# Kernel tuning notes

Hardware: AMD Instinct MI355X
Metric: run time of the kernel (lower is better)

The kernel has to match this reference:

```python
import jax, jax.numpy as jnp
import numpy as np

MAX_SEQ = 20          # text-token prefix length (config.max_seq_length)
NUM_HEADS = 12        # == num_spatial_relations
HEAD_DIM = 64         # 768 / 12
QUADRANTS = (1, 2, 4, 7, 8, 9)
NEG = -10000.0

BS, N_FEAT, D = 128, 182, 768   # N_FEAT = 20 text + 150 ocr/obj + 12 decode steps
R_OCR_OBJ = 150


def setup_inputs() -> dict:
    key = jax.random.key(0)
    ks = jax.random.split(key, 8)
    hidden_states = jax.random.normal(ks[0], (BS, N_FEAT, D), dtype=jnp.float32)
    attention_mask = jnp.where(
        jax.random.uniform(ks[1], (BS, 1, 1, N_FEAT)) < 0.9, 0.0, NEG
    ).astype(jnp.float32)
    # binary spatial relation adjacency (bs, R, R, 12)
    spatial_adj_matrix = jax.random.randint(
        ks[2], (BS, R_OCR_OBJ, R_OCR_OBJ, NUM_HEADS), 0, 2
    ).astype(jnp.float32)
    scale = 0.02
    Wq = jax.random.normal(ks[3], (D, D), dtype=jnp.float32) * scale
    Wk = jax.random.normal(ks[4], (D, D), dtype=jnp.float32) * scale
    Wv = jax.random.normal(ks[5], (D, D), dtype=jnp.float32) * scale
    bq = jnp.zeros((D,), jnp.float32)
    bk = jnp.zeros((D,), jnp.float32)
    bv = jnp.zeros((D,), jnp.float32)
    return {
        "hidden_states": hidden_states,
        "attention_mask": attention_mask,
        "spatial_adj_matrix": spatial_adj_matrix,
        "Wq": Wq, "bq": bq, "Wk": Wk, "bk": bk, "Wv": Wv, "bv": bv,
    }


def _spatial_additive_mask(spatial_adj_matrix, num_features, dtype):
    """Builds (bs, heads, N, N) additive mask in {0, -10000}, faithful to the
    sequential ones-fill / adjacency-copy / quadrant-zero / (1-m)*-10000 / permute."""
    bs, R = spatial_adj_matrix.shape[0], spatial_adj_matrix.shape[1]
    S = MAX_SEQ
    m = jnp.ones((bs, num_features, num_features, NUM_HEADS), dtype)
    m = m.at[:, S:S + R, S:S + R, :].set(spatial_adj_matrix.astype(dtype))
    for quad in QUADRANTS:  # num_spatial_relations == num_heads, so all head channels
        if quad == 1:
            m = m.at[:, :S, :S, :].set(0.0)
        elif quad == 2:
            m = m.at[:, :S, S:S + R, :].set(0.0)
        elif quad == 4:
            m = m.at[:, S:S + R, :S, :].set(0.0)
        elif quad == 7:
            m = m.at[:, S + R:, :S, :].set(0.0)
        elif quad == 8:
            m = m.at[:, S + R:, S:S + R, :].set(0.0)
        elif quad == 9:
            m = m.at[:, S + R:, S + R:, :].set(0.0)
    return jnp.transpose((1.0 - m) * NEG, (0, 3, 1, 2))  # (bs, H, N, N)


def _heads(x, bs, n):
    return jnp.transpose(x.reshape(bs, n, NUM_HEADS, HEAD_DIM), (0, 2, 1, 3))


def reference(hidden_states, attention_mask, spatial_adj_matrix,
              Wq, bq, Wk, bk, Wv, bv):
    bs, n, _ = hidden_states.shape
    spatial = _spatial_additive_mask(spatial_adj_matrix, n, hidden_states.dtype)
    # combined additive mask in {0, -10000}; attention_mask broadcasts (bs,1,1,N)
    combined = jnp.minimum(attention_mask, spatial)
    # 1.0 where a query row has at least one attendable key, else 0.0
    entity_probs_mask = (jnp.max(combined, axis=-1, keepdims=True) + 10000.0) / 10000.0

    q = _heads(hidden_states @ Wq.T + bq, bs, n)  # (bs, H, N, d)
    k = _heads(hidden_states @ Wk.T + bk, bs, n)
    v = _heads(hidden_states @ Wv.T + bv, bs, n)

    scores = jnp.einsum('bhqd,bhkd->bhqk', q, k) / 8.0 + combined  # sqrt(64)=8
    probs = jax.nn.softmax(scores, axis=-1) * entity_probs_mask
    ctx = jnp.einsum('bhqk,bhkd->bhqd', probs, v)
    ctx = jnp.transpose(ctx, (0, 2, 1, 3)).reshape(bs, n, NUM_HEADS * HEAD_DIM)
    return ctx
```

## Files before the change

### kernel.cpp

```cpp
#include <hip/hip_runtime.h>
#include <hip/hip_bf16.h>

#define NBS   128
#define NF    182
#define NP    192
#define DMODEL 768
#define NH    12
#define HDIM  64
#define SEQT  20
#define ROCR  150

typedef __attribute__((ext_vector_type(4))) float  f32x4;
typedef __attribute__((ext_vector_type(8))) short  s16x8;
typedef __attribute__((ext_vector_type(4))) unsigned int u32x4;
using bf16 = __hip_bfloat16;

#define SB()    __builtin_amdgcn_sched_barrier(0)
#define BAR()   __builtin_amdgcn_s_barrier()

__device__ __forceinline__ void gload_lds16(const void* g, void* l) {
    auto gp = (const __attribute__((address_space(1))) unsigned int*)((unsigned long long)g);
    auto lp = (__attribute__((address_space(3))) unsigned int*)(unsigned int)((unsigned long long)l);
    __builtin_amdgcn_global_load_lds(gp, lp, 16, 0, 0);
}

#define CVT_BLOCKS 9600
__global__ __launch_bounds__(256) void prep(
    const float* __restrict__ hs,
    const float* __restrict__ Wq, const float* __restrict__ Wk, const float* __restrict__ Wv,
    const float* __restrict__ adj,
    bf16* __restrict__ hsb, bf16* __restrict__ Wb2,
    unsigned long long* __restrict__ bits)
{
    __shared__ float tile[ROCR * NH];
    if (blockIdx.x < CVT_BLOCKS) {
        const size_t HT = (size_t)NBS * NF * DMODEL / 8;
        const size_t WT = 3ull * DMODEL * DMODEL / 8;
        size_t i = (size_t)blockIdx.x * 256 + threadIdx.x;
        if (i >= HT + WT) return;
        const float* src; bf16* dst;
        if (i < HT) {
            size_t e = i * 8; src = hs + e; dst = hsb + e;
        } else {
            size_t e = (i - HT) * 8;
            int R = (int)(e / DMODEL), c = (int)(e % DMODEL);
            int h = R / 192, t2 = (R % 192) / 64, r0 = R % 64;
            src = (t2 == 0 ? Wq : t2 == 1 ? Wk : Wv) + (size_t)(h * 64 + r0) * DMODEL + c;
            dst = Wb2 + e;
        }
        float4 a = *reinterpret_cast<const float4*>(src);
        float4 b = *reinterpret_cast<const float4*>(src + 4);
        union { s16x8 v; bf16 h8[8]; } u;
        u.h8[0] = __float2bfloat16(a.x); u.h8[1] = __float2bfloat16(a.y);
        u.h8[2] = __float2bfloat16(a.z); u.h8[3] = __float2bfloat16(a.w);
        u.h8[4] = __float2bfloat16(b.x); u.h8[5] = __float2bfloat16(b.y);
        u.h8[6] = __float2bfloat16(b.z); u.h8[7] = __float2bfloat16(b.w);
        *reinterpret_cast<s16x8*>(dst) = u.v;
    } else {
        const int pb = blockIdx.x - CVT_BLOCKS;
        const int b = pb / ROCR, r = pb - b * ROCR;
        const int tid = threadIdx.x, lane = tid & 63, w = tid >> 6;
        const float* src = adj + ((size_t)b * ROCR + r) * (ROCR * NH);
        for (int i = tid; i < ROCR * NH; i += 256) tile[i] = src[i];
        __syncthreads();
        for (int c = w; c < NH * 3; c += 4) {
            int hh = c / 3, wd = c - hh * 3;
            int k = wd * 64 + lane;
            int j = k - SEQT;
            bool v = false;
            if (j >= 0 && j < ROCR) v = (tile[j * NH + hh] > 0.5f);
            unsigned long long m = __ballot(v);
            if (lane == 0) bits[(((size_t)b * NH + hh) * ROCR + r) * 3 + wd] = m;
        }
    }
}

#define KO2   0
#define VTO2  24576
#define QO3   49152

__global__ __launch_bounds__(256, 2) void fused_qkv_attn(
    const bf16* __restrict__ hsb, const bf16* __restrict__ Wb2,
    const float* __restrict__ bq, const float* __restrict__ bk, const float* __restrict__ bv,
    const float* __restrict__ amask,
    const unsigned long long* __restrict__ bits,
    float* __restrict__ out)
{
    __shared__ char L[73728];
    const int tid  = threadIdx.x;
    const int lane = tid & 63;
    const int wid  = tid >> 6;
    const int wr = wid >> 1, wc = wid & 1;
    const int lm = lane & 15, lg = lane >> 4;

    const int flat = blockIdx.x;
    const int wgid = (flat & 7) * 192 + (flat >> 3);
    const int b = wgid / NH, h = wgid - b * NH;

    float* obase = out + (size_t)b * NF * DMODEL + h * HDIM;

    unsigned long long aw0, aw1, aw2;
    {
        int k0 = lane, k1 = 64 + lane, k2 = 128 + lane;
        aw0 = __ballot(amask[b * NF + k0] == 0.0f);
        aw1 = __ballot(amask[b * NF + k1] == 0.0f);
        aw2 = __ballot((k2 < NF) && (amask[b * NF + k2] == 0.0f));
    }
    for (int i = tid; i < 12 * 64; i += 256)
        obase[(size_t)(170 + (i >> 6)) * DMODEL + (i & 63)] = 0.f;

    const char* gA = (const char*)(hsb + (size_t)b * NF * DMODEL);
    const char* gW = (const char*)(Wb2 + (size_t)h * 192 * DMODEL);

    f32x4 acc[6][6];
    #pragma unroll
    for (int i = 0; i < 6; ++i)
        #pragma unroll
        for (int j = 0; j < 6; ++j) acc[i][j] = (f32x4){0.f, 0.f, 0.f, 0.f};

    const int srow4 = tid >> 2, sch4 = tid & 3;

    auto ST = [&](int kt, int bsel) {
        char* dA = L + bsel * 24576;
        char* dW = dA + 12288;
        #pragma unroll
        for (int it = 0; it < 3; ++it) {
            int row = it * 64 + srow4;
            int lc = sch4 ^ ((row >> 1) & 3);
            size_t go = (size_t)row * 1536 + (size_t)kt * 64 + lc * 16;
            int o = row * 64 + sch4 * 16;
            gload_lds16(gA + go, dA + o);
            gload_lds16(gW + go, dW + o);
        }
    };
    auto CP = [&](int bsel) {
        const char* Ab = L + bsel * 24576;
        const char* Wp = Ab + 12288;
        s16x8 af[6], bf6[6];
        #pragma unroll
        for (int mi = 0; mi < 6; ++mi) {
            int r = 96 * wr + 16 * mi + lm;
            af[mi] = *reinterpret_cast<const s16x8*>(Ab + r * 64 + ((lg ^ ((r >> 1) & 3)) << 4));
        }
        #pragma unroll
        for (int ni = 0; ni < 6; ++ni) {
            int r = 96 * wc + 16 * ni + lm;
            bf6[ni] = *reinterpret_cast<const s16x8*>(Wp + r * 64 + ((lg ^ ((r >> 1) & 3)) << 4));
        }
        __builtin_amdgcn_s_setprio(1);
        #pragma unroll
        for (int mi = 0; mi < 6; ++mi)
            #pragma unroll
            for (int ni = 0; ni < 6; ++ni)
                acc[mi][ni] = __builtin_amdgcn_mfma_f32_16x16x32_bf16(af[mi], bf6[ni], acc[mi][ni], 0, 0, 0);
        __builtin_amdgcn_s_setprio(0);
    };

    ST(0, 0);
    ST(1, 1);
    ST(2, 2);
    for (int t = 0; t < 24; ++t) {
        if (t <= 21)      { asm volatile("s_waitcnt vmcnt(12)" ::: "memory"); }
        else if (t == 22) { asm volatile("s_waitcnt vmcnt(6)"  ::: "memory"); }
        else              { asm volatile("s_waitcnt vmcnt(0)"  ::: "memory"); }
        SB(); BAR(); SB();
        CP(t % 3);
        SB(); BAR();
        if (t + 3 < 24) ST(t + 3, t % 3);
    }
    BAR();

    float bias6[6];
    #pragma unroll
    for (int ni = 0; ni < 6; ++ni) {
        int c = 96 * wc + 16 * ni + lm;
        int whichc = c >> 6, cc = c & 63;
        const float* bp = (whichc == 0) ? bq : (whichc == 1) ? bk : bv;
        bias6[ni] = bp[h * 64 + cc];
    }
    #pragma unroll
    for (int mi = 0; mi < 6; ++mi) {
        #pragma unroll
        for (int ni = 0; ni < 6; ++ni) {
            int c = 96 * wc + 16 * ni + lm;
            int row0 = 96 * wr + 16 * mi + 4 * lg;
            if (c < 64) {
                #pragma unroll
                for (int j = 0; j < 4; ++j) {
                    int row = row0 + j;
                    bf16 hv = __float2bfloat16((acc[mi][ni][j] + bias6[ni]) * 0.125f);
                    *reinterpret_cast<unsigned short*>(L + QO3 + row * 128 + ((2 * c) ^ ((row & 7) << 4))) =
                        *reinterpret_cast<unsigned short*>(&hv);
                }
            } else if (c < 128) {
                int cc = c - 64;
                #pragma unroll
                for (int j = 0; j < 4; ++j) {
                    int row = row0 + j;
                    bf16 hv = __float2bfloat16(acc[mi][ni][j] + bias6[ni]);
                    *reinterpret_cast<unsigned short*>(L + KO2 + row * 128 + ((2 * cc) ^ ((row & 7) << 4))) =
                        *reinterpret_cast<unsigned short*>(&hv);
                }
            } else {
                int d = c - 128;
                if (row0 + 3 < NF) {
                    union { unsigned long long u8; bf16 h[4]; } pk;
                    pk.h[0] = __float2bfloat16(acc[mi][ni][0] + bias6[ni]);
                    pk.h[1] = __float2bfloat16(acc[mi][ni][1] + bias6[ni]);
                    pk.h[2] = __float2bfloat16(acc[mi][ni][2] + bias6[ni]);
                    pk.h[3] = __float2bfloat16(acc[mi][ni][3] + bias6[ni]);
                    *reinterpret_cast<unsigned long long*>(L + VTO2 + d * 384 + ((2 * row0) ^ ((d & 7) << 4))) = pk.u8;
                } else {
                    #pragma unroll
                    for (int j = 0; j < 4; ++j) {
                        int row = row0 + j;
                        if (row < NF) {
                            bf16 hv = __float2bfloat16(acc[mi][ni][j] + bias6[ni]);
                            *reinterpret_cast<unsigned short*>(L + VTO2 + d * 384 + ((2 * row) ^ ((d & 7) << 4))) =
                                *reinterpret_cast<unsigned short*>(&hv);
                        }
                    }
                }
            }
        }
    }
    for (int i = tid; i < 64 * 10; i += 256) {
        int d = i / 10, k2 = NF + (i - d * 10);
        *reinterpret_cast<unsigned short*>(L + VTO2 + d * 384 + ((2 * k2) ^ ((d & 7) << 4))) = 0;
    }
    __syncthreads();

    s16x8 qf[3][2];
    #pragma unroll
    for (int bi = 0; bi < 3; ++bi) {
        int band = wid + 4 * bi;
        int qrow = ((band < 11) ? band * 16 : 0) + lm;
        const char* qb = L + QO3 + qrow * 128;
        int sq = (qrow & 7) << 4;
        qf[bi][0] = *reinterpret_cast<const s16x8*>(qb + ((lg * 16) ^ sq));
        qf[bi][1] = *reinterpret_cast<const s16x8*>(qb + ((64 + lg * 16) ^ sq));
    }

    const unsigned long long* bbase = bits + ((size_t)b * NH + h) * ROCR * 3;
    const unsigned long long DEC = 0xFFFull << 42;

    #pragma unroll
    for (int bi = 0; bi < 3; ++bi) {
        const int band = wid + 4 * bi;
        if (band >= 11) continue;
        const int q0 = band * 16;

        const int qrow = q0 + lm;
        unsigned long long mw0, mw1, mw2;
        if (qrow < SEQT) {
            mw0 = 0; mw1 = 0; mw2 = DEC & aw2;
        } else {
            const unsigned long long* bp = bbase + (size_t)(qrow - SEQT) * 3;
            mw0 = bp[0] & aw0;
            mw1 = bp[1] & aw1;
            mw2 = (bp[2] | DEC) & aw2;
        }

        f32x4 sacc[12];
        #pragma unroll
        for (int t = 0; t < 12; ++t) sacc[t] = (f32x4){0.f, 0.f, 0.f, 0.f};
        #pragma unroll
        for (int t = 0; t < 12; ++t) {
            int key = t * 16 + lm;
            const char* kb = L + KO2 + key * 128;
            int sw = (key & 7) << 4;
            s16x8 kf0 = *reinterpret_cast<const s16x8*>(kb + ((lg * 16) ^ sw));
            s16x8 kf1 = *reinterpret_cast<const s16x8*>(kb + ((64 + lg * 16) ^ sw));
            sacc[t] = __builtin_amdgcn_mfma_f32_16x16x32_bf16(kf0, qf[bi][0], sacc[t], 0, 0, 0);
            sacc[t] = __builtin_amdgcn_mfma_f32_16x16x32_bf16(kf1, qf[bi][1], sacc[t], 0, 0, 0);
        }

        float mx = -3.0e38f;
        #pragma unroll
        for (int t = 0; t < 12; ++t) {
            unsigned long long w = (t < 4) ? mw0 : (t < 8) ? mw1 : mw2;
            #pragma unroll
            for (int j = 0; j < 4; ++j) {
                int sh = ((t & 3) << 4) + 4 * lg + j;
                float s = sacc[t][j];
                s = ((w >> sh) & 1ull) ? s : -3.0e38f;
                sacc[t][j] = s;
                mx = fmaxf(mx, s);
            }
        }
        mx = fmaxf(mx, __shfl_xor(mx, 16));
        mx = fmaxf(mx, __shfl_xor(mx, 32));
        float sum = 0.f;
        #pragma unroll
        for (int t = 0; t < 12; ++t)
            #pragma unroll
            for (int j = 0; j < 4; ++j) {
                float e = (sacc[t][j] > -1.0e37f) ? __expf(sacc[t][j] - mx) : 0.f;
                sacc[t][j] = e;
                sum += e;
            }
        sum += __shfl_xor(sum, 16);
        sum += __shfl_xor(sum, 32);
        float scl = (mx > -1.0e37f) ? 1.0f / sum : 0.f;

        unsigned int p0[12], p1[12];
        #pragma unroll
        for (int t = 0; t < 12; ++t) {
            bf16 b0 = __float2bfloat16(sacc[t][0] * scl);
            bf16 b1 = __float2bfloat16(sacc[t][1] * scl);
            bf16 b2 = __float2bfloat16(sacc[t][2] * scl);
            bf16 b3 = __float2bfloat16(sacc[t][3] * scl);
            p0[t] = (unsigned int)*reinterpret_cast<unsigned short*>(&b0)
                  | ((unsigned int)*reinterpret_cast<unsigned short*>(&b1) << 16);
            p1[t] = (unsigned int)*reinterpret_cast<unsigned short*>(&b2)
                  | ((unsigned int)*reinterpret_cast<unsigned short*>(&b3) << 16);
        }

        f32x4 oacc[4];
        #pragma unroll
        for (int t = 0; t < 4; ++t) oacc[t] = (f32x4){0.f, 0.f, 0.f, 0.f};
        const bool hi = (lg & 1);
        #pragma unroll
        for (int ks = 0; ks < 6; ++ks) {
            unsigned int A0 = p0[2 * ks],     A1 = p1[2 * ks];
            unsigned int B0 = p0[2 * ks + 1], B1 = p1[2 * ks + 1];
            unsigned int u0 = __shfl_xor(A0, 16), u1 = __shfl_xor(A1, 16);
            unsigned int v0 = __shfl_xor(B0, 16), v1 = __shfl_xor(B1, 16);
            unsigned int hA0 = hi ? u0 : A0, hA1 = hi ? u1 : A1;
            unsigned int hA2 = hi ? A0 : u0, hA3 = hi ? A1 : u1;
            unsigned int hB0 = hi ? v0 : B0, hB1 = hi ? v1 : B1;
            unsigned int hB2 = hi ? B0 : v0, hB3 = hi ? B1 : v1;
            unsigned int xA0 = __shfl_xor(hA0, 32), xA1 = __shfl_xor(hA1, 32);
            unsigned int xA2 = __shfl_xor(hA2, 32), xA3 = __shfl_xor(hA3, 32);
            unsigned int xB0 = __shfl_xor(hB0, 32), xB1 = __shfl_xor(hB1, 32);
            unsigned int xB2 = __shfl_xor(hB2, 32), xB3 = __shfl_xor(hB3, 32);
            u32x4 f;
            if (lg == 0)      f = (u32x4){hA0, hA1, hA2, hA3};
            else if (lg == 1) f = (u32x4){xA0, xA1, xA2, xA3};
            else if (lg == 2) f = (u32x4){xB0, xB1, xB2, xB3};
            else              f = (u32x4){hB0, hB1, hB2, hB3};
            s16x8 pa;
            __builtin_memcpy(&pa, &f, 16);
            #pragma unroll
            for (int t2 = 0; t2 < 4; ++t2) {
                int d = t2 * 16 + lm;
                s16x8 vf = *reinterpret_cast<const s16x8*>(L + VTO2 + d * 384 + ((ks * 64 + lg * 16) ^ ((d & 7) << 4)));
                oacc[t2] = __builtin_amdgcn_mfma_f32_16x16x32_bf16(pa, vf, oacc[t2], 0, 0, 0);
            }
        }
        #pragma unroll
        for (int j = 0; j < 4; ++j) {
            int row = q0 + lg * 4 + j;
            if (row < 170) {
                #pragma unroll
                for (int t2 = 0; t2 < 4; ++t2)
                    obase[(size_t)row * DMODEL + t2 * 16 + lm] = oacc[t2][j];
            }
        }
    }
}

extern "C" void kernel_launch(void* const* d_in, const int* in_sizes, int n_in,
                              void* d_out, int out_size, void* d_ws, size_t ws_size,
                              hipStream_t stream)
{
    const float* hs    = (const float*)d_in[0];
    const float* amask = (const float*)d_in[1];
    const float* adj   = (const float*)d_in[2];
    const float* Wq    = (const float*)d_in[3];
    const float* bq    = (const float*)d_in[4];
    const float* Wk    = (const float*)d_in[5];
    const float* bk    = (const float*)d_in[6];
    const float* Wv    = (const float*)d_in[7];
    const float* bv    = (const float*)d_in[8];
    float* out = (float*)d_out;

    char* ws = (char*)d_ws;
    bf16* Wb2 = (bf16*)ws;
    unsigned long long* bits = (unsigned long long*)(ws + 3538944);
    bf16* hsb = (bf16*)(ws + 3538944 + 5529600);

    prep<<<dim3(CVT_BLOCKS + ROCR * NBS), 256, 0, stream>>>(hs, Wq, Wk, Wv, adj, hsb, Wb2, bits);
    fused_qkv_attn<<<dim3(NBS * NH), 256, 0, stream>>>(hsb, Wb2, bq, bk, bv, amask, bits, out);
}
```

Measured before the change: 202.3 us.

## Use 12 waves per block for fused QKV projection and attention

Raises the fused QKV+attention block from 4 to 12 waves (768 threads, 1 block per CU). In the projection GEMM each wave now owns a 48x64 tile in a 4x3 grid, with the column group matching Q, K or V. Each wave loads one row of each staged tile and works one 16-row query band in attention, so there is no loop over three bands. This cuts per-wave accumulator registers and serial work per wave and spreads latency hiding across more waves. The cost is 1 block per CU instead of 2, and one wave sits idle during the attention phase.

```diff
diff --git a/kernel.cpp b/kernel.cpp
--- a/kernel.cpp
+++ b/kernel.cpp
@@ -79,7 +79,7 @@
 #define VTO2  24576
 #define QO3   49152
 
-__global__ __launch_bounds__(256, 2) void fused_qkv_attn(
+__global__ __launch_bounds__(768, 1) void fused_qkv_attn(
     const bf16* __restrict__ hsb, const bf16* __restrict__ Wb2,
     const float* __restrict__ bq, const float* __restrict__ bk, const float* __restrict__ bv,
     const float* __restrict__ amask,
@@ -90,7 +90,7 @@
     const int tid  = threadIdx.x;
     const int lane = tid & 63;
     const int wid  = tid >> 6;
-    const int wr = wid >> 1, wc = wid & 1;
+    const int wr = wid / 3, wc = wid - wr * 3;
     const int lm = lane & 15, lg = lane >> 4;
 
     const int flat = blockIdx.x;
@@ -106,53 +106,47 @@
         aw1 = __ballot(amask[b * NF + k1] == 0.0f);
         aw2 = __ballot((k2 < NF) && (amask[b * NF + k2] == 0.0f));
     }
-    for (int i = tid; i < 12 * 64; i += 256)
-        obase[(size_t)(170 + (i >> 6)) * DMODEL + (i & 63)] = 0.f;
+    obase[(size_t)(170 + (tid >> 6)) * DMODEL + (tid & 63)] = 0.f;
 
     const char* gA = (const char*)(hsb + (size_t)b * NF * DMODEL);
     const char* gW = (const char*)(Wb2 + (size_t)h * 192 * DMODEL);
 
-    f32x4 acc[6][6];
+    f32x4 acc[3][4];
     #pragma unroll
-    for (int i = 0; i < 6; ++i)
-        #pragma unroll
-        for (int j = 0; j < 6; ++j) acc[i][j] = (f32x4){0.f, 0.f, 0.f, 0.f};
-
-    const int srow4 = tid >> 2, sch4 = tid & 3;
+    for (int i = 0; i < 3; ++i)
+        #pragma unroll
+        for (int j = 0; j < 4; ++j) acc[i][j] = (f32x4){0.f, 0.f, 0.f, 0.f};
+
+    const int srow = tid >> 2, sch = tid & 3;
 
     auto ST = [&](int kt, int bsel) {
         char* dA = L + bsel * 24576;
-        char* dW = dA + 12288;
-        #pragma unroll
-        for (int it = 0; it < 3; ++it) {
-            int row = it * 64 + srow4;
-            int lc = sch4 ^ ((row >> 1) & 3);
-            size_t go = (size_t)row * 1536 + (size_t)kt * 64 + lc * 16;
-            int o = row * 64 + sch4 * 16;
-            gload_lds16(gA + go, dA + o);
-            gload_lds16(gW + go, dW + o);
-        }
+        int lc = sch ^ ((srow >> 1) & 3);
+        size_t go = (size_t)srow * 1536 + (size_t)kt * 64 + lc * 16;
+        int o = srow * 64 + sch * 16;
+        gload_lds16(gA + go, dA + o);
+        gload_lds16(gW + go, dA + 12288 + o);
     };
     auto CP = [&](int bsel) {
         const char* Ab = L + bsel * 24576;
         const char* Wp = Ab + 12288;
-        s16x8 af[6], bf6[6];
-        #pragma unroll
-        for (int mi = 0; mi < 6; ++mi) {
-            int r = 96 * wr + 16 * mi + lm;
+        s16x8 af[3], bf4[4];
+        #pragma unroll
+        for (int mi = 0; mi < 3; ++mi) {
+            int r = 48 * wr + 16 * mi + lm;
             af[mi] = *reinterpret_cast<const s16x8*>(Ab + r * 64 + ((lg ^ ((r >> 1) & 3)) << 4));
         }
         #pragma unroll
-        for (int ni = 0; ni < 6; ++ni) {
-            int r = 96 * wc + 16 * ni + lm;
-            bf6[ni] = *reinterpret_cast<const s16x8*>(Wp + r * 64 + ((lg ^ ((r >> 1) & 3)) << 4));
+        for (int ni = 0; ni < 4; ++ni) {
+            int r = 64 * wc + 16 * ni + lm;
+            bf4[ni] = *reinterpret_cast<const s16x8*>(Wp + r * 64 + ((lg ^ ((r >> 1) & 3)) << 4));
         }
         __builtin_amdgcn_s_setprio(1);
         #pragma unroll
-        for (int mi = 0; mi < 6; ++mi)
-            #pragma unroll
-            for (int ni = 0; ni < 6; ++ni)
-                acc[mi][ni] = __builtin_amdgcn_mfma_f32_16x16x32_bf16(af[mi], bf6[ni], acc[mi][ni], 0, 0, 0);
+        for (int mi = 0; mi < 3; ++mi)
+            #pragma unroll
+            for (int ni = 0; ni < 4; ++ni)
+                acc[mi][ni] = __builtin_amdgcn_mfma_f32_16x16x32_bf16(af[mi], bf4[ni], acc[mi][ni], 0, 0, 0);
         __builtin_amdgcn_s_setprio(0);
     };
 
@@ -160,9 +154,9 @@
     ST(1, 1);
     ST(2, 2);
     for (int t = 0; t < 24; ++t) {
-        if (t <= 21)      { asm volatile("s_waitcnt vmcnt(12)" ::: "memory"); }
-        else if (t == 22) { asm volatile("s_waitcnt vmcnt(6)"  ::: "memory"); }
-        else              { asm volatile("s_waitcnt vmcnt(0)"  ::: "memory"); }
+        if (t <= 21)      { asm volatile("s_waitcnt vmcnt(4)" ::: "memory"); }
+        else if (t == 22) { asm volatile("s_waitcnt vmcnt(2)" ::: "memory"); }
+        else              { asm volatile("s_waitcnt vmcnt(0)" ::: "memory"); }
         SB(); BAR(); SB();
         CP(t % 3);
         SB(); BAR();
@@ -170,84 +164,79 @@
     }
     BAR();
 
-    float bias6[6];
-    #pragma unroll
-    for (int ni = 0; ni < 6; ++ni) {
-        int c = 96 * wc + 16 * ni + lm;
-        int whichc = c >> 6, cc = c & 63;
-        const float* bp = (whichc == 0) ? bq : (whichc == 1) ? bk : bv;
-        bias6[ni] = bp[h * 64 + cc];
-    }
-    #pragma unroll
-    for (int mi = 0; mi < 6; ++mi) {
-        #pragma unroll
-        for (int ni = 0; ni < 6; ++ni) {
-            int c = 96 * wc + 16 * ni + lm;
-            int row0 = 96 * wr + 16 * mi + 4 * lg;
-            if (c < 64) {
-                #pragma unroll
-                for (int j = 0; j < 4; ++j) {
-                    int row = row0 + j;
-                    bf16 hv = __float2bfloat16((acc[mi][ni][j] + bias6[ni]) * 0.125f);
-                    *reinterpret_cast<unsigned short*>(L + QO3 + row * 128 + ((2 * c) ^ ((row & 7) << 4))) =
-                        *reinterpret_cast<unsigned short*>(&hv);
-                }
-            } else if (c < 128) {
-                int cc = c - 64;
-                #pragma unroll
-                for (int j = 0; j < 4; ++j) {
-                    int row = row0 + j;
-                    bf16 hv = __float2bfloat16(acc[mi][ni][j] + bias6[ni]);
-                    *reinterpret_cast<unsigned short*>(L + KO2 + row * 128 + ((2 * cc) ^ ((row & 7) << 4))) =
-                        *reinterpret_cast<unsigned short*>(&hv);
-                }
-            } else {
-                int d = c - 128;
-                if (row0 + 3 < NF) {
-                    union { unsigned long long u8; bf16 h[4]; } pk;
-                    pk.h[0] = __float2bfloat16(acc[mi][ni][0] + bias6[ni]);
-                    pk.h[1] = __float2bfloat16(acc[mi][ni][1] + bias6[ni]);
-                    pk.h[2] = __float2bfloat16(acc[mi][ni][2] + bias6[ni]);
-                    pk.h[3] = __float2bfloat16(acc[mi][ni][3] + bias6[ni]);
-                    *reinterpret_cast<unsigned long long*>(L + VTO2 + d * 384 + ((2 * row0) ^ ((d & 7) << 4))) = pk.u8;
-                } else {
+    {
+        const float* bp = (wc == 0) ? bq : (wc == 1) ? bk : bv;
+        float bias4[4];
+        #pragma unroll
+        for (int ni = 0; ni < 4; ++ni) bias4[ni] = bp[h * 64 + 16 * ni + lm];
+
+        #pragma unroll
+        for (int mi = 0; mi < 3; ++mi) {
+            int row0 = 48 * wr + 16 * mi + 4 * lg;
+            #pragma unroll
+            for (int ni = 0; ni < 4; ++ni) {
+                int c = 16 * ni + lm;
+                if (wc == 0) {
                     #pragma unroll
                     for (int j = 0; j < 4; ++j) {
                         int row = row0 + j;
-                        if (row < NF) {
-                            bf16 hv = __float2bfloat16(acc[mi][ni][j] + bias6[ni]);
-                            *reinterpret_cast<unsigned short*>(L + VTO2 + d * 384 + ((2 * row) ^ ((d & 7) << 4))) =
+                        if (row < 176) {
+                            bf16 hv = __float2bfloat16((acc[mi][ni][j] + bias4[ni]) * 0.125f);
+                            *reinterpret_cast<unsigned short*>(L + QO3 + row * 128 + ((2 * c) ^ ((row & 7) << 4))) =
                                 *reinterpret_cast<unsigned short*>(&hv);
                         }
                     }
+                } else if (wc == 1) {
+                    #pragma unroll
+                    for (int j = 0; j < 4; ++j) {
+                        int row = row0 + j;
+                        bf16 hv = __float2bfloat16(acc[mi][ni][j] + bias4[ni]);
+                        *reinterpret_cast<unsigned short*>(L + KO2 + row * 128 + ((2 * c) ^ ((row & 7) << 4))) =
+                            *reinterpret_cast<unsigned short*>(&hv);
+                    }
+                } else {
+                    int d = c;
+                    if (row0 + 3 < NF) {
+                        union { unsigned long long u8; bf16 h4[4]; } pk;
+                        pk.h4[0] = __float2bfloat16(acc[mi][ni][0] + bias4[ni]);
+                        pk.h4[1] = __float2bfloat16(acc[mi][ni][1] + bias4[ni]);
+                        pk.h4[2] = __float2bfloat16(acc[mi][ni][2] + bias4[ni]);
+                        pk.h4[3] = __float2bfloat16(acc[mi][ni][3] + bias4[ni]);
+                        *reinterpret_cast<unsigned long long*>(L + VTO2 + d * 384 + ((2 * row0) ^ ((d & 7) << 4))) = pk.u8;
+                    } else {
+                        #pragma unroll
+                        for (int j = 0; j < 4; ++j) {
+                            int row = row0 + j;
+                            if (row < NF) {
+                                bf16 hv = __float2bfloat16(acc[mi][ni][j] + bias4[ni]);
+                                *reinterpret_cast<unsigned short*>(L + VTO2 + d * 384 + ((2 * row) ^ ((d & 7) << 4))) =
+                                    *reinterpret_cast<unsigned short*>(&hv);
+                            }
+                        }
+                    }
                 }
             }
         }
     }
-    for (int i = tid; i < 64 * 10; i += 256) {
+    for (int i = tid; i < 64 * 10; i += 768) {
         int d = i / 10, k2 = NF + (i - d * 10);
         *reinterpret_cast<unsigned short*>(L + VTO2 + d * 384 + ((2 * k2) ^ ((d & 7) << 4))) = 0;
     }
     __syncthreads();
 
-    s16x8 qf[3][2];
-    #pragma unroll
-    for (int bi = 0; bi < 3; ++bi) {
-        int band = wid + 4 * bi;
-        int qrow = ((band < 11) ? band * 16 : 0) + lm;
+    const int band = (wid < 11) ? wid : 0;
+    s16x8 qf0, qf1;
+    {
+        int qrow = band * 16 + lm;
         const char* qb = L + QO3 + qrow * 128;
         int sq = (qrow & 7) << 4;
-        qf[bi][0] = *reinterpret_cast<const s16x8*>(qb + ((lg * 16) ^ sq));
-        qf[bi][1] = *reinterpret_cast<const s16x8*>(qb + ((64 + lg * 16) ^ sq));
-    }
-
-    const unsigned long long* bbase = bits + ((size_t)b * NH + h) * ROCR * 3;
-    const unsigned long long DEC = 0xFFFull << 42;
-
-    #pragma unroll
-    for (int bi = 0; bi < 3; ++bi) {
-        const int band = wid + 4 * bi;
-        if (band >= 11) continue;
+        qf0 = *reinterpret_cast<const s16x8*>(qb + ((lg * 16) ^ sq));
+        qf1 = *reinterpret_cast<const s16x8*>(qb + ((64 + lg * 16) ^ sq));
+    }
+
+    if (wid < 11) {
+        const unsigned long long* bbase = bits + ((size_t)b * NH + h) * ROCR * 3;
+        const unsigned long long DEC = 0xFFFull << 42;
         const int q0 = band * 16;
 
         const int qrow = q0 + lm;
@@ -271,8 +260,8 @@
             int sw = (key & 7) << 4;
             s16x8 kf0 = *reinterpret_cast<const s16x8*>(kb + ((lg * 16) ^ sw));
             s16x8 kf1 = *reinterpret_cast<const s16x8*>(kb + ((64 + lg * 16) ^ sw));
-            sacc[t] = __builtin_amdgcn_mfma_f32_16x16x32_bf16(kf0, qf[bi][0], sacc[t], 0, 0, 0);
-            sacc[t] = __builtin_amdgcn_mfma_f32_16x16x32_bf16(kf1, qf[bi][1], sacc[t], 0, 0, 0);
+            sacc[t] = __builtin_amdgcn_mfma_f32_16x16x32_bf16(kf0, qf0, sacc[t], 0, 0, 0);
+            sacc[t] = __builtin_amdgcn_mfma_f32_16x16x32_bf16(kf1, qf1, sacc[t], 0, 0, 0);
         }
 
         float mx = -3.0e38f;
@@ -381,5 +370,5 @@
     bf16* hsb = (bf16*)(ws + 3538944 + 5529600);
 
     prep<<<dim3(CVT_BLOCKS + ROCR * NBS), 256, 0, stream>>>(hs, Wq, Wk, Wv, adj, hsb, Wb2, bits);
-    fused_qkv_attn<<<dim3(NBS * NH), 256, 0, stream>>>(hsb, Wb2, bq, bk, bv, amask, bits, out);
+    fused_qkv_attn<<<dim3(NBS * NH), 768, 0, stream>>>(hsb, Wb2, bq, bk, bv, amask, bits, out);
 }
```

Measured after the change: 218.8 us. +8.2%, slower.
